# Optimization experiments

Hardware: AMD Instinct MI355X
Metric: run time of the kernel (lower is better)

## Reference

```python
import jax, jax.numpy as jnp
import numpy as np

B, N, T, F = 8, 512, 1024, 8


def setup_inputs() -> dict:
    key = jax.random.key(0)
    k1, k2, k3 = jax.random.split(key, 3)
    inp = jax.random.normal(k1, (B, N, N), dtype=jnp.float32)
    # bin edges must be monotonically increasing (torch.searchsorted requirement)
    bins = jnp.sort(jax.random.normal(k2, (B, T), dtype=jnp.float32) * 2.0, axis=-1)
    weights = jax.random.uniform(k3, (B, N, N, F), dtype=jnp.float32)
    return {"input": inp, "bins": bins, "weights": weights}


def reference(input, bins, weights):
    """Faithful port of batch_histogram: batched weighted histogram via
    sort + searchsorted + cumsum + gather (same math as the torch original)."""
    b, n, _ = input.shape
    t = bins.shape[1]
    f = weights.shape[-1]

    flat = input.reshape(b, n * n)                       # [B, N*N]
    sorted_idx = jnp.argsort(flat, axis=-1)              # [B, N*N]
    sorted_vals = jnp.take_along_axis(flat, sorted_idx, axis=-1)

    # counts[b, j] = number of sorted values strictly below bins[b, j]
    counts = jax.vmap(lambda sv, bn: jnp.searchsorted(sv, bn, side="left"))(sorted_vals, bins)  # [B, T]

    w = weights.reshape(b, n * n, f)                     # [B, N*N, F]
    sorted_w = jnp.take_along_axis(w, sorted_idx[:, :, None], axis=1)  # [B, N*N, F]
    cumsum_w = jnp.cumsum(sorted_w, axis=1)              # [B, N*N, F]

    idx = jnp.clip(counts - 1, 0)                        # [B, T]
    bin_cs = jnp.take_along_axis(cumsum_w, jnp.broadcast_to(idx[:, :, None], (b, t, f)), axis=1)
    padded = jnp.concatenate([jnp.zeros((b, 1, f), dtype=cumsum_w.dtype), bin_cs], axis=1)
    return jnp.diff(padded, axis=1)                      # [B, T, F]
```

## Files before the change

### kernel.cpp

```cpp
#include <hip/hip_runtime.h>
#include <hip/hip_fp16.h>
#include <stdint.h>

#define BB 8
#define NSQ 262144
#define TT 1024
#define FF 8
#define CH 9
#define PP 128
#define EPB 2048
#define ITERS 2
#define NONE_U32 0xFFFFFFFFu

using ull = unsigned long long;

__device__ inline ull pack_key(float v, unsigned idx) {
    unsigned u = __float_as_uint(v);
    unsigned key = (u & 0x80000000u) ? ~u : (u | 0x80000000u);
    return ((ull)key << 32) | (ull)idx;
}

__device__ inline unsigned pkrtz(float a, float b) {
    auto h = __builtin_amdgcn_cvt_pkrtz(a, b);
    unsigned u; __builtin_memcpy(&u, &h, 4); return u;
}
__device__ inline float2 unpk(unsigned u) {
    __half2 h; __builtin_memcpy(&h, &u, 4);
    return __half22float2(h);
}

__device__ inline void tree5(float v, const float* __restrict__ cf,
                             int& lo_out, int& hi_out) {
    bool s0 = cf[0] <= v;
    float m1 = s0 ? cf[2] : cf[1];
    bool s1 = m1 <= v;
    float a2 = s1 ? cf[4] : cf[3];
    float b2 = s1 ? cf[6] : cf[5];
    float m2 = s0 ? b2 : a2;
    bool s2 = m2 <= v;
    float a3 = s2 ? cf[8]  : cf[7];
    float b3 = s2 ? cf[10] : cf[9];
    float c3 = s2 ? cf[12] : cf[11];
    float d3 = s2 ? cf[14] : cf[13];
    float e3 = s1 ? b3 : a3;
    float f3 = s1 ? d3 : c3;
    float m3 = s0 ? f3 : e3;
    bool s3 = m3 <= v;
    float a4 = s3 ? cf[16] : cf[15];
    float b4 = s3 ? cf[18] : cf[17];
    float c4 = s3 ? cf[20] : cf[19];
    float d4 = s3 ? cf[22] : cf[21];
    float e4 = s3 ? cf[24] : cf[23];
    float f4 = s3 ? cf[26] : cf[25];
    float g4 = s3 ? cf[28] : cf[27];
    float h4 = s3 ? cf[30] : cf[29];
    float i4 = s2 ? b4 : a4;
    float j4 = s2 ? d4 : c4;
    float k4 = s2 ? f4 : e4;
    float l4 = s2 ? h4 : g4;
    float n4 = s1 ? j4 : i4;
    float o4 = s1 ? l4 : k4;
    float m4 = s0 ? o4 : n4;
    bool s4 = m4 <= v;
    int lo = 0, hi = TT, m;
    m = (lo + hi) >> 1; lo = s0 ? m + 1 : lo; hi = s0 ? hi : m;
    m = (lo + hi) >> 1; lo = s1 ? m + 1 : lo; hi = s1 ? hi : m;
    m = (lo + hi) >> 1; lo = s2 ? m + 1 : lo; hi = s2 ? hi : m;
    m = (lo + hi) >> 1; lo = s3 ? m + 1 : lo; hi = s3 ? hi : m;
    m = (lo + hi) >> 1; lo = s4 ? m + 1 : lo; hi = s4 ? hi : m;
    lo_out = lo; hi_out = hi;
}

__global__ __launch_bounds__(256, 4) void histo_kernel(
    const float* __restrict__ inp, const float* __restrict__ bins,
    const float* __restrict__ wts,
    __half* __restrict__ partF,
    unsigned short* __restrict__ partC,
    ull* __restrict__ partMin)
{
    __shared__ uint4 sVal[EPB];
    __shared__ unsigned scnt[TT];
    __shared__ unsigned sPfx[TT];
    float* sbins   = (float*)sVal;
    ull* sMinW     = (ull*)(sVal + 256);
    unsigned* sWs  = (unsigned*)(sVal + 258);

    int b = blockIdx.x / PP, p = blockIdx.x % PP;
    int tid = threadIdx.x;
    int lane = tid & 63, wv = tid >> 6;

    for (int i = tid; i < TT; i += 256) { sbins[i] = bins[b * TT + i]; scnt[i] = 0u; }
    __syncthreads();

    float cf[31];
    cf[0] = sbins[512]; cf[1] = sbins[256]; cf[2] = sbins[768];
    #pragma unroll
    for (int k = 0; k < 4; ++k)  cf[3 + k]  = sbins[128 + 256 * k];
    #pragma unroll
    for (int k = 0; k < 8; ++k)  cf[7 + k]  = sbins[64 + 128 * k];
    #pragma unroll
    for (int k = 0; k < 16; ++k) cf[15 + k] = sbins[32 + 64 * k];

    const float4* inp4 = (const float4*)(inp + (size_t)b * NSQ + (size_t)p * EPB);

    unsigned idrank[ITERS * 4];
    ull lmin = ~0ull;
    #pragma unroll
    for (int it = 0; it < ITERS; ++it) {
        int q = it * 256 + tid;
        float4 v = inp4[q];

        int lo0, hi0, lo1, hi1, lo2, hi2, lo3, hi3;
        tree5(v.x, cf, lo0, hi0);
        tree5(v.y, cf, lo1, hi1);
        tree5(v.z, cf, lo2, hi2);
        tree5(v.w, cf, lo3, hi3);
        #pragma unroll
        for (int lev = 0; lev < 5; ++lev) {
            int m0 = (lo0 + hi0) >> 1, m1 = (lo1 + hi1) >> 1;
            int m2 = (lo2 + hi2) >> 1, m3 = (lo3 + hi3) >> 1;
            float b0 = sbins[m0], b1 = sbins[m1], b2 = sbins[m2], b3 = sbins[m3];
            if (b0 <= v.x) lo0 = m0 + 1; else hi0 = m0;
            if (b1 <= v.y) lo1 = m1 + 1; else hi1 = m1;
            if (b2 <= v.z) lo2 = m2 + 1; else hi2 = m2;
            if (b3 <= v.w) lo3 = m3 + 1; else hi3 = m3;
        }
        if (lo0 < hi0 && sbins[lo0] <= v.x) ++lo0;
        if (lo1 < hi1 && sbins[lo1] <= v.y) ++lo1;
        if (lo2 < hi2 && sbins[lo2] <= v.z) ++lo2;
        if (lo3 < hi3 && sbins[lo3] <= v.w) ++lo3;

        unsigned e0 = (unsigned)(p * EPB + q * 4);
        lmin = min(lmin, pack_key(v.x, e0 + 0));
        lmin = min(lmin, pack_key(v.y, e0 + 1));
        lmin = min(lmin, pack_key(v.z, e0 + 2));
        lmin = min(lmin, pack_key(v.w, e0 + 3));

        idrank[it*4+0] = (lo0 < TT) ? ((unsigned)lo0 << 16) | atomicAdd(&scnt[lo0], 1u) : NONE_U32;
        idrank[it*4+1] = (lo1 < TT) ? ((unsigned)lo1 << 16) | atomicAdd(&scnt[lo1], 1u) : NONE_U32;
        idrank[it*4+2] = (lo2 < TT) ? ((unsigned)lo2 << 16) | atomicAdd(&scnt[lo2], 1u) : NONE_U32;
        idrank[it*4+3] = (lo3 < TT) ? ((unsigned)lo3 << 16) | atomicAdd(&scnt[lo3], 1u) : NONE_U32;
    }

    for (int off = 32; off > 0; off >>= 1) {
        unsigned hi32 = (unsigned)(lmin >> 32), lo32 = (unsigned)(lmin & 0xFFFFFFFFu);
        unsigned ohi = __shfl_down(hi32, off, 64);
        unsigned olo = __shfl_down(lo32, off, 64);
        ull other = ((ull)ohi << 32) | (ull)olo;
        if (other < lmin) lmin = other;
    }
    if (lane == 0) sMinW[wv] = lmin;
    __syncthreads();

    if (tid == 0) {
        ull m = sMinW[0];
        #pragma unroll
        for (int w = 1; w < 4; ++w) { ull t = sMinW[w]; if (t < m) m = t; }
        partMin[(size_t)p * BB + b] = m;
    }

    int t4 = tid * 4;
    unsigned c0 = scnt[t4], c1 = scnt[t4 + 1], c2 = scnt[t4 + 2], c3 = scnt[t4 + 3];
    {
        ushort4 u4 = make_ushort4((unsigned short)c0, (unsigned short)c1,
                                  (unsigned short)c2, (unsigned short)c3);
        ushort4* dst = (ushort4*)(partC + ((size_t)b * PP + p) * TT);
        dst[tid] = u4;
    }
    unsigned l1 = c0 + c1, l2 = l1 + c2, l3 = l2 + c3;
    unsigned s = l3;
    #pragma unroll
    for (int off = 1; off < 64; off <<= 1) {
        unsigned n = __shfl_up(s, off, 64);
        if (lane >= off) s += n;
    }
    if (lane == 63) sWs[wv] = s;
    __syncthreads();
    unsigned wbase = 0;
    #pragma unroll
    for (int w = 0; w < 4; ++w) if (w < wv) wbase += sWs[w];
    unsigned tbase = wbase + s - l3;
    sPfx[t4 + 0] = tbase;
    sPfx[t4 + 1] = tbase + c0;
    sPfx[t4 + 2] = tbase + l1;
    sPfx[t4 + 3] = tbase + l2;
    __syncthreads();

    const float4* wp = (const float4*)(wts + ((size_t)b * NSQ + (size_t)p * EPB) * FF);
    #pragma unroll
    for (int it = 0; it < ITERS; ++it) {
        int q = it * 256 + tid;
        float4 wa0 = wp[(size_t)q*8+0], wb0 = wp[(size_t)q*8+1];
        float4 wa1 = wp[(size_t)q*8+2], wb1 = wp[(size_t)q*8+3];
        float4 wa2 = wp[(size_t)q*8+4], wb2 = wp[(size_t)q*8+5];
        float4 wa3 = wp[(size_t)q*8+6], wb3 = wp[(size_t)q*8+7];
        unsigned v0 = idrank[it*4+0], v1 = idrank[it*4+1];
        unsigned v2 = idrank[it*4+2], v3 = idrank[it*4+3];
        if (v0 != NONE_U32) {
            unsigned slot = sPfx[v0 >> 16] + (v0 & 0xFFFFu);
            sVal[slot] = make_uint4(pkrtz(wa0.x, wa0.y), pkrtz(wa0.z, wa0.w),
                                    pkrtz(wb0.x, wb0.y), pkrtz(wb0.z, wb0.w));
        }
        if (v1 != NONE_U32) {
            unsigned slot = sPfx[v1 >> 16] + (v1 & 0xFFFFu);
            sVal[slot] = make_uint4(pkrtz(wa1.x, wa1.y), pkrtz(wa1.z, wa1.w),
                                    pkrtz(wb1.x, wb1.y), pkrtz(wb1.z, wb1.w));
        }
        if (v2 != NONE_U32) {
            unsigned slot = sPfx[v2 >> 16] + (v2 & 0xFFFFu);
            sVal[slot] = make_uint4(pkrtz(wa2.x, wa2.y), pkrtz(wa2.z, wa2.w),
                                    pkrtz(wb2.x, wb2.y), pkrtz(wb2.z, wb2.w));
        }
        if (v3 != NONE_U32) {
            unsigned slot = sPfx[v3 >> 16] + (v3 & 0xFFFFu);
            sVal[slot] = make_uint4(pkrtz(wa3.x, wa3.y), pkrtz(wa3.z, wa3.w),
                                    pkrtz(wb3.x, wb3.y), pkrtz(wb3.z, wb3.w));
        }
    }
    __syncthreads();

    #pragma unroll
    for (int k = 0; k < 4; ++k) {
        int t = tid + 256 * k;
        unsigned start = sPfx[t];
        unsigned end = start + scnt[t];
        float a0 = 0.f, a1 = 0.f, a2 = 0.f, a3 = 0.f;
        float a4 = 0.f, a5 = 0.f, a6 = 0.f, a7 = 0.f;
        for (unsigned e = start; e < end; ++e) {
            uint4 v = sVal[e];
            float2 f0 = unpk(v.x), f1 = unpk(v.y);
            float2 f2 = unpk(v.z), f3 = unpk(v.w);
            a0 += f0.x; a1 += f0.y; a2 += f1.x; a3 += f1.y;
            a4 += f2.x; a5 += f2.y; a6 += f3.x; a7 += f3.y;
        }
        size_t pb = ((size_t)b * FF * PP + p) * TT + t;
        partF[pb + 0 * (size_t)PP * TT] = __float2half(a0);
        partF[pb + 1 * (size_t)PP * TT] = __float2half(a1);
        partF[pb + 2 * (size_t)PP * TT] = __float2half(a2);
        partF[pb + 3 * (size_t)PP * TT] = __float2half(a3);
        partF[pb + 4 * (size_t)PP * TT] = __float2half(a4);
        partF[pb + 5 * (size_t)PP * TT] = __float2half(a5);
        partF[pb + 6 * (size_t)PP * TT] = __float2half(a6);
        partF[pb + 7 * (size_t)PP * TT] = __float2half(a7);
    }
}

__global__ __launch_bounds__(256) void reduce_kernel(
    const __half* __restrict__ partF, const unsigned short* __restrict__ partC,
    float* __restrict__ red)
{
    int idx = blockIdx.x * 256 + threadIdx.x;
    if (idx >= BB * CH * 512) return;
    int bc = idx >> 9;
    int t2 = idx & 511;
    int b = bc / CH, ch = bc - b * CH;
    float s0 = 0.f, s1 = 0.f;
    if (ch < FF) {
        const unsigned* src = (const unsigned*)(partF + (((size_t)b * FF + ch) * PP) * TT) + t2;
        #pragma unroll 8
        for (int p = 0; p < PP; ++p) {
            float2 f = unpk(src[(size_t)p * 512]);
            s0 += f.x; s1 += f.y;
        }
    } else {
        const unsigned* src = (const unsigned*)(partC + ((size_t)b * PP) * TT) + t2;
        #pragma unroll 8
        for (int p = 0; p < PP; ++p) {
            unsigned u = src[(size_t)p * 512];
            s0 += (float)(u & 0xFFFFu);
            s1 += (float)(u >> 16);
        }
    }
    *((float2*)(red + (size_t)bc * TT) + t2) = make_float2(s0, s1);
}

__global__ __launch_bounds__(256) void scan_kernel(
    const float* __restrict__ red, const ull* __restrict__ partMin,
    const float* __restrict__ wts, float* __restrict__ out)
{
    int b = blockIdx.x / FF, f = blockIdx.x % FF;
    int tid = threadIdx.x;
    int lane = tid & 63, wv = tid >> 6;
    __shared__ float sC[TT];
    __shared__ float sW[TT];
    __shared__ float sTot[2][4];
    __shared__ ull sMin2[2];
    __shared__ unsigned sMinIdx;

    ull m = ~0ull;
    if (tid < PP) m = partMin[(size_t)tid * BB + b];
    for (int off = 32; off > 0; off >>= 1) {
        unsigned hi32 = (unsigned)(m >> 32), lo32 = (unsigned)(m & 0xFFFFFFFFu);
        unsigned ohi = __shfl_down(hi32, off, 64);
        unsigned olo = __shfl_down(lo32, off, 64);
        ull other = ((ull)ohi << 32) | (ull)olo;
        if (other < m) m = other;
    }
    if (lane == 0 && wv < 2) sMin2[wv] = m;

    int t4 = tid * 4;
    float4 c4 = *(const float4*)(red + ((size_t)b * CH + FF) * TT + t4);
    float cl1 = c4.x + c4.y, cl2 = cl1 + c4.z, cl3 = cl2 + c4.w;
    float cs = cl3;
    #pragma unroll
    for (int off = 1; off < 64; off <<= 1) {
        float n = __shfl_up(cs, off, 64);
        if (lane >= off) cs += n;
    }
    if (lane == 63) sTot[0][wv] = cs;

    float4 w4 = *(const float4*)(red + ((size_t)b * CH + f) * TT + t4);
    float wl1 = w4.x + w4.y, wl2 = wl1 + w4.z, wl3 = wl2 + w4.w;
    float ws = wl3;
    #pragma unroll
    for (int off = 1; off < 64; off <<= 1) {
        float n = __shfl_up(ws, off, 64);
        if (lane >= off) ws += n;
    }
    if (lane == 63) sTot[1][wv] = ws;
    __syncthreads();

    if (tid == 0) {
        ull mm = (sMin2[0] < sMin2[1]) ? sMin2[0] : sMin2[1];
        sMinIdx = (unsigned)(mm & 0xFFFFFFFFu);
    }
    float cbase = 0.f, wbase = 0.f;
    #pragma unroll
    for (int w = 0; w < 4; ++w) if (w < wv) { cbase += sTot[0][w]; wbase += sTot[1][w]; }
    float cexcl = cbase + cs - cl3;
    float wexcl = wbase + ws - wl3;
    sC[t4 + 0] = cexcl + c4.x;
    sC[t4 + 1] = cexcl + cl1;
    sC[t4 + 2] = cexcl + cl2;
    sC[t4 + 3] = cexcl + cl3;
    sW[t4 + 0] = wexcl + w4.x;
    sW[t4 + 1] = wexcl + wl1;
    sW[t4 + 2] = wexcl + wl2;
    sW[t4 + 3] = wexcl + wl3;
    __syncthreads();

    float wmin = wts[((size_t)b * NSQ + sMinIdx) * FF + f];
    #pragma unroll
    for (int k = 0; k < 4; ++k) {
        int t = t4 + k;
        float scj = sC[t], Cj = sW[t];
        float csj = (scj == 0.f) ? wmin : Cj;
        float csjm1;
        if (t == 0) csjm1 = 0.f;
        else {
            float scp = sC[t - 1], Cp = sW[t - 1];
            csjm1 = (scp == 0.f) ? wmin : Cp;
        }
        out[((size_t)b * TT + t) * FF + f] = csj - csjm1;
    }
}

extern "C" void kernel_launch(void* const* d_in, const int* in_sizes, int n_in,
                              void* d_out, int out_size, void* d_ws, size_t ws_size,
                              hipStream_t stream)
{
    const float* inp  = (const float*)d_in[0];
    const float* bins = (const float*)d_in[1];
    const float* wts  = (const float*)d_in[2];
    float* out = (float*)d_out;

    char* w = (char*)d_ws;
    __half* partF = (__half*)w;          w += (size_t)BB * FF * PP * TT * 2;
    unsigned short* partC = (unsigned short*)w; w += (size_t)BB * PP * TT * 2;
    ull* partMin = (ull*)w;              w += (size_t)PP * BB * 8;
    float* red = (float*)w;

    histo_kernel<<<dim3(BB * PP), dim3(256), 0, stream>>>(
        inp, bins, wts, partF, partC, partMin);
    reduce_kernel<<<dim3((BB * CH * 512 + 255) / 256), dim3(256), 0, stream>>>(
        partF, partC, red);
    scan_kernel<<<dim3(BB * FF), dim3(256), 0, stream>>>(
        red, partMin, wts, out);
}
```

Baseline: 43.87 us.

## Use 512-thread blocks with one float4 per thread in histogram kernel

Doubles the histo block size to 512 threads so each thread handles one float4 of input instead of two. Each thread then owns two bins instead of four during the scan and accumulation. The input load is issued before the bins staging to overlap latency, and the partial sums are written as packed half2 pairs. This aims to raise parallelism and cut per-thread serial work, at the cost of tighter register limits from the (512,8) launch bounds and more scan synchronization across 8 waves.

After: 48.97 us. 11.6% more time.

```diff
diff --git a/kernel.cpp b/kernel.cpp
--- a/kernel.cpp
+++ b/kernel.cpp
@@ -9,7 +9,6 @@
 #define CH 9
 #define PP 128
 #define EPB 2048
-#define ITERS 2
 #define NONE_U32 0xFFFFFFFFu
 
 using ull = unsigned long long;
@@ -71,7 +70,7 @@
     lo_out = lo; hi_out = hi;
 }
 
-__global__ __launch_bounds__(256, 4) void histo_kernel(
+__global__ __launch_bounds__(512, 8) void histo_kernel(
     const float* __restrict__ inp, const float* __restrict__ bins,
     const float* __restrict__ wts,
     __half* __restrict__ partF,
@@ -83,13 +82,18 @@
     __shared__ unsigned sPfx[TT];
     float* sbins   = (float*)sVal;
     ull* sMinW     = (ull*)(sVal + 256);
-    unsigned* sWs  = (unsigned*)(sVal + 258);
+    unsigned* sWs  = (unsigned*)(sVal + 260);
 
     int b = blockIdx.x / PP, p = blockIdx.x % PP;
     int tid = threadIdx.x;
     int lane = tid & 63, wv = tid >> 6;
 
-    for (int i = tid; i < TT; i += 256) { sbins[i] = bins[b * TT + i]; scnt[i] = 0u; }
+    const float4* inp4 = (const float4*)(inp + (size_t)b * NSQ + (size_t)p * EPB);
+    const float4* wp   = (const float4*)(wts + ((size_t)b * NSQ + (size_t)p * EPB) * FF);
+
+    float4 v = inp4[tid];
+
+    for (int i = tid; i < TT; i += 512) { sbins[i] = bins[b * TT + i]; scnt[i] = 0u; }
     __syncthreads();
 
     float cf[31];
@@ -101,15 +105,9 @@
     #pragma unroll
     for (int k = 0; k < 16; ++k) cf[15 + k] = sbins[32 + 64 * k];
 
-    const float4* inp4 = (const float4*)(inp + (size_t)b * NSQ + (size_t)p * EPB);
-
-    unsigned idrank[ITERS * 4];
+    unsigned idrank[4];
     ull lmin = ~0ull;
-    #pragma unroll
-    for (int it = 0; it < ITERS; ++it) {
-        int q = it * 256 + tid;
-        float4 v = inp4[q];
-
+    {
         int lo0, hi0, lo1, hi1, lo2, hi2, lo3, hi3;
         tree5(v.x, cf, lo0, hi0);
         tree5(v.y, cf, lo1, hi1);
@@ -130,16 +128,16 @@
         if (lo2 < hi2 && sbins[lo2] <= v.z) ++lo2;
         if (lo3 < hi3 && sbins[lo3] <= v.w) ++lo3;
 
-        unsigned e0 = (unsigned)(p * EPB + q * 4);
+        unsigned e0 = (unsigned)(p * EPB + tid * 4);
         lmin = min(lmin, pack_key(v.x, e0 + 0));
         lmin = min(lmin, pack_key(v.y, e0 + 1));
         lmin = min(lmin, pack_key(v.z, e0 + 2));
         lmin = min(lmin, pack_key(v.w, e0 + 3));
 
-        idrank[it*4+0] = (lo0 < TT) ? ((unsigned)lo0 << 16) | atomicAdd(&scnt[lo0], 1u) : NONE_U32;
-        idrank[it*4+1] = (lo1 < TT) ? ((unsigned)lo1 << 16) | atomicAdd(&scnt[lo1], 1u) : NONE_U32;
-        idrank[it*4+2] = (lo2 < TT) ? ((unsigned)lo2 << 16) | atomicAdd(&scnt[lo2], 1u) : NONE_U32;
-        idrank[it*4+3] = (lo3 < TT) ? ((unsigned)lo3 << 16) | atomicAdd(&scnt[lo3], 1u) : NONE_U32;
+        idrank[0] = (lo0 < TT) ? ((unsigned)lo0 << 16) | atomicAdd(&scnt[lo0], 1u) : NONE_U32;
+        idrank[1] = (lo1 < TT) ? ((unsigned)lo1 << 16) | atomicAdd(&scnt[lo1], 1u) : NONE_U32;
+        idrank[2] = (lo2 < TT) ? ((unsigned)lo2 << 16) | atomicAdd(&scnt[lo2], 1u) : NONE_U32;
+        idrank[3] = (lo3 < TT) ? ((unsigned)lo3 << 16) | atomicAdd(&scnt[lo3], 1u) : NONE_U32;
     }
 
     for (int off = 32; off > 0; off >>= 1) {
@@ -155,20 +153,19 @@
     if (tid == 0) {
         ull m = sMinW[0];
         #pragma unroll
-        for (int w = 1; w < 4; ++w) { ull t = sMinW[w]; if (t < m) m = t; }
+        for (int w = 1; w < 8; ++w) { ull t = sMinW[w]; if (t < m) m = t; }
         partMin[(size_t)p * BB + b] = m;
     }
 
-    int t4 = tid * 4;
-    unsigned c0 = scnt[t4], c1 = scnt[t4 + 1], c2 = scnt[t4 + 2], c3 = scnt[t4 + 3];
+    int t2 = tid * 2;
+    unsigned c0 = scnt[t2], c1 = scnt[t2 + 1];
     {
-        ushort4 u4 = make_ushort4((unsigned short)c0, (unsigned short)c1,
-                                  (unsigned short)c2, (unsigned short)c3);
-        ushort4* dst = (ushort4*)(partC + ((size_t)b * PP + p) * TT);
-        dst[tid] = u4;
-    }
-    unsigned l1 = c0 + c1, l2 = l1 + c2, l3 = l2 + c3;
-    unsigned s = l3;
+        ushort2 u2 = make_ushort2((unsigned short)c0, (unsigned short)c1);
+        ushort2* dst = (ushort2*)(partC + ((size_t)b * PP + p) * TT);
+        dst[tid] = u2;
+    }
+    unsigned l1 = c0 + c1;
+    unsigned s = l1;
     #pragma unroll
     for (int off = 1; off < 64; off <<= 1) {
         unsigned n = __shfl_up(s, off, 64);
@@ -178,70 +175,53 @@
     __syncthreads();
     unsigned wbase = 0;
     #pragma unroll
-    for (int w = 0; w < 4; ++w) if (w < wv) wbase += sWs[w];
-    unsigned tbase = wbase + s - l3;
-    sPfx[t4 + 0] = tbase;
-    sPfx[t4 + 1] = tbase + c0;
-    sPfx[t4 + 2] = tbase + l1;
-    sPfx[t4 + 3] = tbase + l2;
-    __syncthreads();
-
-    const float4* wp = (const float4*)(wts + ((size_t)b * NSQ + (size_t)p * EPB) * FF);
-    #pragma unroll
-    for (int it = 0; it < ITERS; ++it) {
-        int q = it * 256 + tid;
-        float4 wa0 = wp[(size_t)q*8+0], wb0 = wp[(size_t)q*8+1];
-        float4 wa1 = wp[(size_t)q*8+2], wb1 = wp[(size_t)q*8+3];
-        float4 wa2 = wp[(size_t)q*8+4], wb2 = wp[(size_t)q*8+5];
-        float4 wa3 = wp[(size_t)q*8+6], wb3 = wp[(size_t)q*8+7];
-        unsigned v0 = idrank[it*4+0], v1 = idrank[it*4+1];
-        unsigned v2 = idrank[it*4+2], v3 = idrank[it*4+3];
-        if (v0 != NONE_U32) {
-            unsigned slot = sPfx[v0 >> 16] + (v0 & 0xFFFFu);
-            sVal[slot] = make_uint4(pkrtz(wa0.x, wa0.y), pkrtz(wa0.z, wa0.w),
-                                    pkrtz(wb0.x, wb0.y), pkrtz(wb0.z, wb0.w));
-        }
-        if (v1 != NONE_U32) {
-            unsigned slot = sPfx[v1 >> 16] + (v1 & 0xFFFFu);
-            sVal[slot] = make_uint4(pkrtz(wa1.x, wa1.y), pkrtz(wa1.z, wa1.w),
-                                    pkrtz(wb1.x, wb1.y), pkrtz(wb1.z, wb1.w));
-        }
-        if (v2 != NONE_U32) {
-            unsigned slot = sPfx[v2 >> 16] + (v2 & 0xFFFFu);
-            sVal[slot] = make_uint4(pkrtz(wa2.x, wa2.y), pkrtz(wa2.z, wa2.w),
-                                    pkrtz(wb2.x, wb2.y), pkrtz(wb2.z, wb2.w));
-        }
-        if (v3 != NONE_U32) {
-            unsigned slot = sPfx[v3 >> 16] + (v3 & 0xFFFFu);
-            sVal[slot] = make_uint4(pkrtz(wa3.x, wa3.y), pkrtz(wa3.z, wa3.w),
-                                    pkrtz(wb3.x, wb3.y), pkrtz(wb3.z, wb3.w));
-        }
-    }
+    for (int w = 0; w < 8; ++w) if (w < wv) wbase += sWs[w];
+    unsigned tbase = wbase + s - l1;
+    sPfx[t2]     = tbase;
+    sPfx[t2 + 1] = tbase + c0;
     __syncthreads();
 
     #pragma unroll
     for (int k = 0; k < 4; ++k) {
-        int t = tid + 256 * k;
-        unsigned start = sPfx[t];
-        unsigned end = start + scnt[t];
-        float a0 = 0.f, a1 = 0.f, a2 = 0.f, a3 = 0.f;
-        float a4 = 0.f, a5 = 0.f, a6 = 0.f, a7 = 0.f;
-        for (unsigned e = start; e < end; ++e) {
-            uint4 v = sVal[e];
-            float2 f0 = unpk(v.x), f1 = unpk(v.y);
-            float2 f2 = unpk(v.z), f3 = unpk(v.w);
-            a0 += f0.x; a1 += f0.y; a2 += f1.x; a3 += f1.y;
-            a4 += f2.x; a5 += f2.y; a6 += f3.x; a7 += f3.y;
-        }
-        size_t pb = ((size_t)b * FF * PP + p) * TT + t;
-        partF[pb + 0 * (size_t)PP * TT] = __float2half(a0);
-        partF[pb + 1 * (size_t)PP * TT] = __float2half(a1);
-        partF[pb + 2 * (size_t)PP * TT] = __float2half(a2);
-        partF[pb + 3 * (size_t)PP * TT] = __float2half(a3);
-        partF[pb + 4 * (size_t)PP * TT] = __float2half(a4);
-        partF[pb + 5 * (size_t)PP * TT] = __float2half(a5);
-        partF[pb + 6 * (size_t)PP * TT] = __float2half(a6);
-        partF[pb + 7 * (size_t)PP * TT] = __float2half(a7);
+        unsigned vr = idrank[k];
+        size_t e = (size_t)(tid * 4 + k);
+        float4 wa = wp[e * 2 + 0];
+        float4 wb = wp[e * 2 + 1];
+        if (vr != NONE_U32) {
+            unsigned slot = sPfx[vr >> 16] + (vr & 0xFFFFu);
+            sVal[slot] = make_uint4(pkrtz(wa.x, wa.y), pkrtz(wa.z, wa.w),
+                                    pkrtz(wb.x, wb.y), pkrtz(wb.z, wb.w));
+        }
+    }
+    __syncthreads();
+
+    float a00=0.f,a01=0.f,a02=0.f,a03=0.f,a04=0.f,a05=0.f,a06=0.f,a07=0.f;
+    float a10=0.f,a11=0.f,a12=0.f,a13=0.f,a14=0.f,a15=0.f,a16=0.f,a17=0.f;
+    unsigned mid = tbase + c0, end = mid + c1;
+    for (unsigned e = tbase; e < mid; ++e) {
+        uint4 u = sVal[e];
+        float2 f0 = unpk(u.x), f1 = unpk(u.y), f2 = unpk(u.z), f3 = unpk(u.w);
+        a00 += f0.x; a01 += f0.y; a02 += f1.x; a03 += f1.y;
+        a04 += f2.x; a05 += f2.y; a06 += f3.x; a07 += f3.y;
+    }
+    for (unsigned e = mid; e < end; ++e) {
+        uint4 u = sVal[e];
+        float2 f0 = unpk(u.x), f1 = unpk(u.y), f2 = unpk(u.z), f3 = unpk(u.w);
+        a10 += f0.x; a11 += f0.y; a12 += f1.x; a13 += f1.y;
+        a14 += f2.x; a15 += f2.y; a16 += f3.x; a17 += f3.y;
+    }
+    {
+        size_t pb = ((size_t)b * FF * PP + p) * TT + t2;
+        unsigned* o = (unsigned*)(partF + pb);
+        const size_t st = (size_t)PP * TT / 2;
+        o[0*st] = pkrtz(a00, a10);
+        o[1*st] = pkrtz(a01, a11);
+        o[2*st] = pkrtz(a02, a12);
+        o[3*st] = pkrtz(a03, a13);
+        o[4*st] = pkrtz(a04, a14);
+        o[5*st] = pkrtz(a05, a15);
+        o[6*st] = pkrtz(a06, a16);
+        o[7*st] = pkrtz(a07, a17);
     }
 }
 
@@ -370,7 +350,7 @@
     ull* partMin = (ull*)w;              w += (size_t)PP * BB * 8;
     float* red = (float*)w;
 
-    histo_kernel<<<dim3(BB * PP), dim3(256), 0, stream>>>(
+    histo_kernel<<<dim3(BB * PP), dim3(512), 0, stream>>>(
         inp, bins, wts, partF, partC, partMin);
     reduce_kernel<<<dim3((BB * CH * 512 + 255) / 256), dim3(256), 0, stream>>>(
         partF, partC, red);
```
